# Optimization experiments

Hardware: AMD Instinct MI355X
Metric: run time of the kernel (lower is better)

Reference implementation:

```python
import jax, jax.numpy as jnp
import numpy as np

N_NODES = 50000
N_EDGES = 800000
D_IN = 128
D_HID = 128
D_OUT = 1
N_LAYERS = 3


def _sage_conv(x, src, dst, Wl, bl, Wr):
    # PyG SAGEConv (mean aggr): out = lin_l(mean_{j in N(i)} x_j) + lin_r(x_i)
    n = x.shape[0]
    msg = x[src]                                              # [E, F] gather
    s = jax.ops.segment_sum(msg, dst, num_segments=n)         # [N, F]
    cnt = jax.ops.segment_sum(jnp.ones((src.shape[0],), x.dtype), dst, num_segments=n)
    mean = s / jnp.maximum(cnt, 1.0)[:, None]
    return mean @ Wl.T + bl + x @ Wr.T


def setup_inputs() -> dict:
    key = jax.random.key(0)
    ks = jax.random.split(key, 2 + 3 * N_LAYERS + 2)
    x = jax.random.normal(ks[0], (N_NODES, D_IN), dtype=jnp.float32)
    edge_index = jax.random.randint(ks[1], (2, N_EDGES), 0, N_NODES, dtype=jnp.int64)
    inp = {"x": x, "edge_index": edge_index}
    dims_in = [D_IN] + [D_HID] * (N_LAYERS - 1)
    for i in range(N_LAYERS):
        fi = dims_in[i]
        sc = 1.0 / np.sqrt(fi)
        inp[f"Wl{i}"] = jax.random.uniform(ks[2 + 3 * i], (D_HID, fi), jnp.float32, -sc, sc)
        inp[f"bl{i}"] = jax.random.uniform(ks[3 + 3 * i], (D_HID,), jnp.float32, -sc, sc)
        inp[f"Wr{i}"] = jax.random.uniform(ks[4 + 3 * i], (D_HID, fi), jnp.float32, -sc, sc)
    sc = 1.0 / np.sqrt(D_HID)
    inp["Wf"] = jax.random.uniform(ks[-2], (D_OUT, D_HID), jnp.float32, -sc, sc)
    inp["bf"] = jax.random.uniform(ks[-1], (D_OUT,), jnp.float32, -sc, sc)
    return inp


def reference(x, edge_index, Wl0, bl0, Wr0, Wl1, bl1, Wr1, Wl2, bl2, Wr2, Wf, bf):
    src, dst = edge_index[0], edge_index[1]
    h = x
    # dropout is identity in eval mode (F.dropout with training=False)
    for Wl, bl, Wr in ((Wl0, bl0, Wr0), (Wl1, bl1, Wr1), (Wl2, bl2, Wr2)):
        h = jax.nn.relu(_sage_conv(h, src, dst, Wl, bl, Wr))
    return h @ Wf.T + bf
```

## Files before the change

kernel.cpp:

```cpp
#include <hip/hip_runtime.h>
#include <hip/hip_bf16.h>


constexpr int NN = 50000;
constexpr int NE = 800000;
constexpr int NTILE = NN / 16;
constexpr int EPB = 4096;
constexpr int NBLK = (NE + EPB - 1) / EPB;
constexpr int NBUCK = 196;
constexpr int BCAP = 6144;
constexpr int PCAP = 6144;
constexpr int GGRID = 512;
constexpr int XBLK = (NN * 128 / 4 + 255) / 256;

using bf16x8 = __attribute__((ext_vector_type(8))) short;
using f32x4  = __attribute__((ext_vector_type(4))) float;

__device__ __forceinline__ unsigned short bf16_rne(float f) {
    unsigned u = __float_as_uint(f);
    unsigned r = (u + 0x7FFFu + ((u >> 16) & 1u)) >> 16;
    return (unsigned short)r;
}
__device__ __forceinline__ float bf16_f(unsigned short h) {
    return __uint_as_float(((unsigned)h) << 16);
}
__device__ __forceinline__ unsigned pack_split(float v) {
    unsigned short hi = bf16_rne(v);
    float r = v - bf16_f(hi);
    unsigned short lo = bf16_rne(r);
    return (((unsigned)hi) << 16) | (unsigned)lo;
}


__global__ __launch_bounds__(256) void k_packinit(const float* __restrict__ x,
        unsigned short* __restrict__ hhi, unsigned short* __restrict__ hlo,
        float* __restrict__ out, const float* __restrict__ bf,
        int* __restrict__ bcnt,
        const float* __restrict__ Wl0, const float* __restrict__ Wr0,
        const float* __restrict__ Wl1, const float* __restrict__ Wr1,
        const float* __restrict__ Wl2, const float* __restrict__ Wr2,
        unsigned short* __restrict__ whi, unsigned short* __restrict__ wlo) {
    if (blockIdx.x >= XBLK) {
        int gi = (blockIdx.x - XBLK) * 256 + threadIdx.x;
        int layer = gi >> 15;
        int i = gi & 32767;
        const float* Wl = (layer == 0) ? Wl0 : (layer == 1) ? Wl1 : Wl2;
        const float* Wr = (layer == 0) ? Wr0 : (layer == 1) ? Wr1 : Wr2;
        int c = i >> 8;
        int k = i & 255;
        float v = (k < 128) ? Wl[c * 128 + k] : Wr[c * 128 + (k - 128)];
        unsigned short hi = bf16_rne(v);
        whi[gi] = hi;
        wlo[gi] = bf16_rne(v - bf16_f(hi));
        return;
    }
    int i = blockIdx.x * blockDim.x + threadIdx.x;
    constexpr int TOT = NN * 128 / 4;
    if (i < TOT) {
        float4 v = ((const float4*)x)[i];
        unsigned p0 = pack_split(v.x), p1 = pack_split(v.y);
        unsigned p2 = pack_split(v.z), p3 = pack_split(v.w);
        uint2 hi, lo;
        hi.x = (p0 >> 16) | (p1 & 0xFFFF0000u);
        hi.y = (p2 >> 16) | (p3 & 0xFFFF0000u);
        lo.x = (p0 & 0xFFFFu) | (p1 << 16);
        lo.y = (p2 & 0xFFFFu) | (p3 << 16);
        ((uint2*)hhi)[i] = hi;
        ((uint2*)hlo)[i] = lo;
    }
    if (i < NN) out[i] = bf[0];
    if (i < 256) bcnt[i] = 0;
    if (i < 128) hhi[(size_t)NN * 128 + i] = 0;
}


__global__ __launch_bounds__(256) void k_build_buckets(const int* __restrict__ ei,
        int* __restrict__ bcnt, unsigned* __restrict__ packed) {
    __shared__ unsigned stage[EPB];
    __shared__ int h[256];
    __shared__ int cur[256];
    int t = threadIdx.x;
    h[t] = 0;
    __syncthreads();
    int e0 = blockIdx.x * EPB;
    int e1 = e0 + EPB; if (e1 > NE) e1 = NE;
    for (int e = e0 + t; e < e1; e += 256) {
        int s = ei[e];
        int d = ei[NE + e];
        stage[e - e0] = ((unsigned)d << 16) | (unsigned)s;
        atomicAdd(&h[d >> 8], 1);
    }
    __syncthreads();
    if (t < NBUCK) cur[t] = t * BCAP + atomicAdd(&bcnt[t], h[t]);
    __syncthreads();
    for (int e = e0 + t; e < e1; e += 256) {
        unsigned r = stage[e - e0];
        int pos = atomicAdd(&cur[r >> 24], 1);
        packed[pos] = r;
    }
}

__global__ __launch_bounds__(256) void k_bucket_csr(const unsigned* __restrict__ packed,
        const int* __restrict__ bcnt, unsigned short* __restrict__ perm,
        int* __restrict__ cnt, int* __restrict__ row_start) {
    __shared__ unsigned recs[BCAP];
    __shared__ unsigned short outs[PCAP];
    __shared__ int cntL[256];
    __shared__ int ws[4];
    __shared__ int totS;
    int b = blockIdx.x;
    int m = bcnt[b];
    if (m > BCAP) m = BCAP;
    int t = threadIdx.x;
    cntL[t] = 0;
    __syncthreads();
    int lo = b * BCAP;
    for (int i = t; i < m; i += 256) {
        unsigned r = packed[lo + i];
        recs[i] = r;
        atomicAdd(&cntL[(r >> 16) & 255], 1);
    }
    __syncthreads();
    int lane = t & 63, wave = t >> 6;
    int orig = cntL[t];
    int pc = (orig + 7) & ~7;
    int v = pc;
    for (int o = 1; o < 64; o <<= 1) { int u = __shfl_up(v, o); if (lane >= o) v += u; }
    if (lane == 63) ws[wave] = v;
    __syncthreads();
    int off = 0;
    for (int w = 0; w < wave; ++w) off += ws[w];
    int st = v + off - pc;
    int node = b * 256 + t;
    if (node < NN) { cnt[node] = orig; row_start[node] = b * PCAP + st; }
    if (t == 255) totS = st + pc;
    __syncthreads();
    cntL[t] = st;
    __syncthreads();
    for (int i = t; i < m; i += 256) {
        unsigned r = recs[i];
        int pos = atomicAdd(&cntL[(r >> 16) & 255], 1);
        outs[pos] = (unsigned short)(r & 0xFFFFu);
    }
    for (int i = st + orig; i < st + pc; ++i) outs[i] = (unsigned short)NN;
    __syncthreads();
    int totp = totS;
    for (int i = t; i < totp; i += 256)
        perm[b * PCAP + i] = outs[i];
}

__global__ __launch_bounds__(256) void k_aggregate(const unsigned short* __restrict__ hhi,
        const int* __restrict__ row_start, const int* __restrict__ cnt,
        const unsigned short* __restrict__ perm,
        unsigned short* __restrict__ shi) {
    int wave = __builtin_amdgcn_readfirstlane(threadIdx.x >> 6);
    int lane = threadIdx.x & 63;
    int node = blockIdx.x * 4 + wave;
    if (node >= NN) return;
    int deg = cnt[node];
    int start = row_start[node];
    int eg = lane >> 4;
    int hsh = (eg & 1) << 4;
    bool egHi = (eg & 2) != 0;
    int c16 = (lane & 15) << 4;
    const char* base = (const char*)hhi;
    float a0=0.f,a1=0.f,a2=0.f,a3=0.f,a4=0.f,a5=0.f,a6=0.f,a7=0.f;
#define ACC8(q) { a0 += __uint_as_float((q).x << 16); a1 += __uint_as_float((q).x & 0xFFFF0000u); \
                  a2 += __uint_as_float((q).y << 16); a3 += __uint_as_float((q).y & 0xFFFF0000u); \
                  a4 += __uint_as_float((q).z << 16); a5 += __uint_as_float((q).z & 0xFFFF0000u); \
                  a6 += __uint_as_float((q).w << 16); a7 += __uint_as_float((q).w & 0xFFFF0000u); }
#define GATH(w) (*(const uint4*)(base + ((size_t)(((w) >> hsh) & 0xFFFFu) << 8) + c16))
    int pdeg = (deg + 7) & ~7;
    const uint4* pp = (const uint4*)(perm + start);
    int j = 0;
    for (; j + 16 <= pdeg; j += 16) {
        uint4 P0 = pp[0], P1 = pp[1]; pp += 2;
        unsigned w0 = egHi ? P0.y : P0.x;
        unsigned w1 = egHi ? P0.w : P0.z;
        unsigned w2 = egHi ? P1.y : P1.x;
        unsigned w3 = egHi ? P1.w : P1.z;
        uint4 q0 = GATH(w0);
        uint4 q1 = GATH(w1);
        uint4 q2 = GATH(w2);
        uint4 q3 = GATH(w3);
        ACC8(q0); ACC8(q1); ACC8(q2); ACC8(q3);
    }
    if (j < pdeg) {
        uint4 P0 = *pp;
        unsigned w0 = egHi ? P0.y : P0.x;
        unsigned w1 = egHi ? P0.w : P0.z;
        uint4 q0 = GATH(w0);
        uint4 q1 = GATH(w1);
        ACC8(q0); ACC8(q1);
    }
#undef GATH
#undef ACC8
    a0 += __shfl_xor(a0, 16); a1 += __shfl_xor(a1, 16);
    a2 += __shfl_xor(a2, 16); a3 += __shfl_xor(a3, 16);
    a4 += __shfl_xor(a4, 16); a5 += __shfl_xor(a5, 16);
    a6 += __shfl_xor(a6, 16); a7 += __shfl_xor(a7, 16);
    a0 += __shfl_xor(a0, 32); a1 += __shfl_xor(a1, 32);
    a2 += __shfl_xor(a2, 32); a3 += __shfl_xor(a3, 32);
    a4 += __shfl_xor(a4, 32); a5 += __shfl_xor(a5, 32);
    a6 += __shfl_xor(a6, 32); a7 += __shfl_xor(a7, 32);
    float inv = 1.0f / (float)(deg > 1 ? deg : 1);
    if (eg == 0) {
        uint4 o;
        o.x = (unsigned)bf16_rne(a0 * inv) | ((unsigned)bf16_rne(a1 * inv) << 16);
        o.y = (unsigned)bf16_rne(a2 * inv) | ((unsigned)bf16_rne(a3 * inv) << 16);
        o.z = (unsigned)bf16_rne(a4 * inv) | ((unsigned)bf16_rne(a5 * inv) << 16);
        o.w = (unsigned)bf16_rne(a6 * inv) | ((unsigned)bf16_rne(a7 * inv) << 16);
        ((uint4*)shi)[(size_t)node * 16 + (lane & 15)] = o;
    }
}

#define GEMM_PROLOG \
    int wave = __builtin_amdgcn_readfirstlane(threadIdx.x >> 6); \
    int lane = threadIdx.x & 63; \
    int row = lane & 15; \
    int kb = lane >> 4; \
    int ct0 = wave * 2; \
    bf16x8 bh[2][8], bl[2][8]; \
    _Pragma("unroll") \
    for (int c = 0; c < 2; ++c) \
        _Pragma("unroll") \
        for (int kc = 0; kc < 8; ++kc) { \
            size_t widx = (size_t)((ct0 + c) * 16 + row) * 256 + kc * 32 + kb * 8; \
            bh[c][kc] = *(const bf16x8*)(Whi + widx); \
            bl[c][kc] = *(const bf16x8*)(Wlo + widx); \
        } \
    float b0 = bias[ct0 * 16 + row]; \
    float b1 = bias[ct0 * 16 + 16 + row];

#define LOADT(AS, AH, AL, t) { \
        size_t rb = (size_t)((t) * 16 + row) * 128 + kb * 8; \
        _Pragma("unroll") \
        for (int kc = 0; kc < 4; ++kc) { \
            AS[kc] = *(const bf16x8*)(Ash + rb + kc * 32); \
            AH[kc] = *(const bf16x8*)(Ahh + rb + kc * 32); \
            AL[kc] = *(const bf16x8*)(Ahl + rb + kc * 32); \
        } }

#define MFMA40(AS, AH, AL) \
        f32x4 acc0 = {0.f, 0.f, 0.f, 0.f}; \
        f32x4 acc1 = {0.f, 0.f, 0.f, 0.f}; \
        _Pragma("unroll") \
        for (int kc = 0; kc < 4; ++kc) { \
            acc0 = __builtin_amdgcn_mfma_f32_16x16x32_bf16(AS[kc], bh[0][kc], acc0, 0, 0, 0); \
            acc0 = __builtin_amdgcn_mfma_f32_16x16x32_bf16(AS[kc], bl[0][kc], acc0, 0, 0, 0); \
            acc1 = __builtin_amdgcn_mfma_f32_16x16x32_bf16(AS[kc], bh[1][kc], acc1, 0, 0, 0); \
            acc1 = __builtin_amdgcn_mfma_f32_16x16x32_bf16(AS[kc], bl[1][kc], acc1, 0, 0, 0); \
        } \
        _Pragma("unroll") \
        for (int kc = 0; kc < 4; ++kc) { \
            acc0 = __builtin_amdgcn_mfma_f32_16x16x32_bf16(AH[kc], bh[0][4 + kc], acc0, 0, 0, 0); \
            acc0 = __builtin_amdgcn_mfma_f32_16x16x32_bf16(AL[kc], bh[0][4 + kc], acc0, 0, 0, 0); \
            acc0 = __builtin_amdgcn_mfma_f32_16x16x32_bf16(AH[kc], bl[0][4 + kc], acc0, 0, 0, 0); \
            acc1 = __builtin_amdgcn_mfma_f32_16x16x32_bf16(AH[kc], bh[1][4 + kc], acc1, 0, 0, 0); \
            acc1 = __builtin_amdgcn_mfma_f32_16x16x32_bf16(AL[kc], bh[1][4 + kc], acc1, 0, 0, 0); \
            acc1 = __builtin_amdgcn_mfma_f32_16x16x32_bf16(AH[kc], bl[1][4 + kc], acc1, 0, 0, 0); \
        }

__global__ __launch_bounds__(256, 2) void k_gemm_ws(
        const unsigned short* __restrict__ Ash,
        const unsigned short* __restrict__ Ahh, const unsigned short* __restrict__ Ahl,
        const unsigned short* __restrict__ Whi, const unsigned short* __restrict__ Wlo,
        const float* __restrict__ bias,
        unsigned short* __restrict__ Ohi, unsigned short* __restrict__ Olo) {
    GEMM_PROLOG
#define STEP(AS, AH, AL, t) { \
        MFMA40(AS, AH, AL) \
        __syncthreads();    \
        int cb0 = ct0 * 16 + row; \
        _Pragma("unroll") \
        for (int r = 0; r < 4; ++r) { \
            size_t ro = (size_t)((t) * 16 + kb * 4 + r) * 128; \
            unsigned p0 = pack_split(fmaxf(acc0[r] + b0, 0.f)); \
            unsigned p1 = pack_split(fmaxf(acc1[r] + b1, 0.f)); \
            Ohi[ro + cb0]      = (unsigned short)(p0 >> 16); \
            Olo[ro + cb0]      = (unsigned short)(p0 & 0xFFFFu); \
            Ohi[ro + cb0 + 16] = (unsigned short)(p1 >> 16); \
            Olo[ro + cb0 + 16] = (unsigned short)(p1 & 0xFFFFu); \
        } }
    bf16x8 sA[4], hA[4], lA[4], sB[4], hB[4], lB[4];
    int t = blockIdx.x;
    LOADT(sA, hA, lA, t)
    int tn = t + GGRID;
    for (;;) {
        if (tn < NTILE) LOADT(sB, hB, lB, tn)
        STEP(sA, hA, lA, t)
        if (tn >= NTILE) break;
        t = tn; tn += GGRID;
        if (tn < NTILE) LOADT(sA, hA, lA, tn)
        STEP(sB, hB, lB, t)
        if (tn >= NTILE) break;
        t = tn; tn += GGRID;
    }
#undef STEP
}

__global__ __launch_bounds__(256, 2) void k_gemm_head(
        const unsigned short* __restrict__ Ash,
        const unsigned short* __restrict__ Ahh, const unsigned short* __restrict__ Ahl,
        const unsigned short* __restrict__ Whi, const unsigned short* __restrict__ Wlo,
        const float* __restrict__ bias, const float* __restrict__ Wf,
        float* __restrict__ out) {
    GEMM_PROLOG
    float w0 = Wf[ct0 * 16 + row];
    float w1 = Wf[ct0 * 16 + 16 + row];
#define HSTEP(AS, AH, AL, t) { \
        MFMA40(AS, AH, AL) \
        float part[4]; \
        _Pragma("unroll") \
        for (int r = 0; r < 4; ++r) \
            part[r] = fmaxf(acc0[r] + b0, 0.f) * w0 + fmaxf(acc1[r] + b1, 0.f) * w1; \
        _Pragma("unroll") \
        for (int o = 1; o < 16; o <<= 1) { \
            _Pragma("unroll") \
            for (int r = 0; r < 4; ++r) part[r] += __shfl_xor(part[r], o); \
        } \
        if (row == 0) { \
            _Pragma("unroll") \
            for (int r = 0; r < 4; ++r) atomicAdd(&out[(t) * 16 + kb * 4 + r], part[r]); \
        } }
    bf16x8 sA[4], hA[4], lA[4], sB[4], hB[4], lB[4];
    int t = blockIdx.x;
    LOADT(sA, hA, lA, t)
    int tn = t + GGRID;
    for (;;) {
        if (tn < NTILE) LOADT(sB, hB, lB, tn)
        HSTEP(sA, hA, lA, t)
        if (tn >= NTILE) break;
        t = tn; tn += GGRID;
        if (tn < NTILE) LOADT(sA, hA, lA, tn)
        HSTEP(sB, hB, lB, t)
        if (tn >= NTILE) break;
        t = tn; tn += GGRID;
    }
#undef HSTEP
}

extern "C" void kernel_launch(void* const* d_in, const int* in_sizes, int n_in,
                              void* d_out, int out_size, void* d_ws, size_t ws_size,
                              hipStream_t stream) {
    const float* x   = (const float*)d_in[0];
    const int*   ei  = (const int*)d_in[1];
    const float* Wl0 = (const float*)d_in[2];
    const float* bl0 = (const float*)d_in[3];
    const float* Wr0 = (const float*)d_in[4];
    const float* Wl1 = (const float*)d_in[5];
    const float* bl1 = (const float*)d_in[6];
    const float* Wr1 = (const float*)d_in[7];
    const float* Wl2 = (const float*)d_in[8];
    const float* bl2 = (const float*)d_in[9];
    const float* Wr2 = (const float*)d_in[10];
    const float* Wf  = (const float*)d_in[11];
    const float* bf  = (const float*)d_in[12];
    float* out = (float*)d_out;

    char* p = (char*)d_ws;
    auto alloc = [&](size_t n) { void* r = (void*)p; p += (n + 255) & ~(size_t)255; return r; };
    int*            bcnt      = (int*)alloc(256 * 4);
    int*            cnt       = (int*)alloc((size_t)NN * 4);
    int*            row_start = (int*)alloc((size_t)NN * 4);
    unsigned short* perm      = (unsigned short*)alloc((size_t)NBUCK * PCAP * 2);
    unsigned short* s_hi      = (unsigned short*)alloc((size_t)(NN + 1) * 128 * 2);
    unsigned short* h_hi      = (unsigned short*)alloc((size_t)(NN + 1) * 128 * 2);
    unsigned short* h_lo      = (unsigned short*)alloc((size_t)(NN + 1) * 128 * 2);
    unsigned short* whi       = (unsigned short*)alloc((size_t)3 * 128 * 256 * 2);
    unsigned short* wlo       = (unsigned short*)alloc((size_t)3 * 128 * 256 * 2);
    unsigned*       packed    = (unsigned*)s_hi;

    dim3 b256(256);
    k_packinit<<<dim3(XBLK + 384), b256, 0, stream>>>(
        x, h_hi, h_lo, out, bf, bcnt,
        Wl0, Wr0, Wl1, Wr1, Wl2, Wr2, whi, wlo);
    k_build_buckets<<<dim3(NBLK), b256, 0, stream>>>(ei, bcnt, packed);
    k_bucket_csr<<<dim3(NBUCK), b256, 0, stream>>>(packed, bcnt, perm, cnt, row_start);

    dim3 gAgg((NN + 3) / 4);
    dim3 gGemm(GGRID);

    k_aggregate<<<gAgg, b256, 0, stream>>>(h_hi, row_start, cnt, perm, s_hi);
    k_gemm_ws<<<gGemm, b256, 0, stream>>>(s_hi, h_hi, h_lo,
                                          whi + 0 * 32768, wlo + 0 * 32768, bl0, h_hi, h_lo);
    k_aggregate<<<gAgg, b256, 0, stream>>>(h_hi, row_start, cnt, perm, s_hi);
    k_gemm_ws<<<gGemm, b256, 0, stream>>>(s_hi, h_hi, h_lo,
                                          whi + 1 * 32768, wlo + 1 * 32768, bl1, h_hi, h_lo);
    k_aggregate<<<gAgg, b256, 0, stream>>>(h_hi, row_start, cnt, perm, s_hi);
    k_gemm_head<<<gGemm, b256, 0, stream>>>(s_hi, h_hi, h_lo,
                                            whi + 2 * 32768, wlo + 2 * 32768, bl2, Wf, out);
}
```

Measured before the change: 284.3 us.

## Split aggregate gather into two feature halves over a persistent grid-stride loop

The aggregation kernel now runs as a persistent grid of fixed size. Each wave walks nodes in a grid-stride loop, processing the 128 features in two 128-byte halves. Within a half, 8 lanes cover the 8 chunks of a row and 8 edge groups handle 8 edges at once, so each wave has more independent edges in flight but gathers narrower rows. The aim is to raise memory-level parallelism and keep a smaller working set of feature data resident in cache per pass. In exchange, the perm/cnt/row_start metadata is read twice and an extra shuffle reduction stage is added.

```diff
diff --git a/kernel.cpp b/kernel.cpp
--- a/kernel.cpp
+++ b/kernel.cpp
@@ -11,6 +11,7 @@
 constexpr int BCAP = 6144;
 constexpr int PCAP = 6144;
 constexpr int GGRID = 512;
+constexpr int AGRID = 2048;
 constexpr int XBLK = (NN * 128 / 4 + 255) / 256;
 
 using bf16x8 = __attribute__((ext_vector_type(8))) short;
@@ -155,63 +156,67 @@
         unsigned short* __restrict__ shi) {
     int wave = __builtin_amdgcn_readfirstlane(threadIdx.x >> 6);
     int lane = threadIdx.x & 63;
-    int node = blockIdx.x * 4 + wave;
-    if (node >= NN) return;
-    int deg = cnt[node];
-    int start = row_start[node];
-    int eg = lane >> 4;
+    int eg = lane >> 3;
+    int cl = lane & 7;
     int hsh = (eg & 1) << 4;
-    bool egHi = (eg & 2) != 0;
-    int c16 = (lane & 15) << 4;
+    int wsel = eg >> 1;
     const char* base = (const char*)hhi;
-    float a0=0.f,a1=0.f,a2=0.f,a3=0.f,a4=0.f,a5=0.f,a6=0.f,a7=0.f;
+#define PICK(P) ((((wsel & 2) ? ((wsel & 1) ? (P).w : (P).z) \
+                              : ((wsel & 1) ? (P).y : (P).x)) >> hsh) & 0xFFFFu)
 #define ACC8(q) { a0 += __uint_as_float((q).x << 16); a1 += __uint_as_float((q).x & 0xFFFF0000u); \
                   a2 += __uint_as_float((q).y << 16); a3 += __uint_as_float((q).y & 0xFFFF0000u); \
                   a4 += __uint_as_float((q).z << 16); a5 += __uint_as_float((q).z & 0xFFFF0000u); \
                   a6 += __uint_as_float((q).w << 16); a7 += __uint_as_float((q).w & 0xFFFF0000u); }
-#define GATH(w) (*(const uint4*)(base + ((size_t)(((w) >> hsh) & 0xFFFFu) << 8) + c16))
-    int pdeg = (deg + 7) & ~7;
-    const uint4* pp = (const uint4*)(perm + start);
-    int j = 0;
-    for (; j + 16 <= pdeg; j += 16) {
-        uint4 P0 = pp[0], P1 = pp[1]; pp += 2;
-        unsigned w0 = egHi ? P0.y : P0.x;
-        unsigned w1 = egHi ? P0.w : P0.z;
-        unsigned w2 = egHi ? P1.y : P1.x;
-        unsigned w3 = egHi ? P1.w : P1.z;
-        uint4 q0 = GATH(w0);
-        uint4 q1 = GATH(w1);
-        uint4 q2 = GATH(w2);
-        uint4 q3 = GATH(w3);
-        ACC8(q0); ACC8(q1); ACC8(q2); ACC8(q3);
-    }
-    if (j < pdeg) {
-        uint4 P0 = *pp;
-        unsigned w0 = egHi ? P0.y : P0.x;
-        unsigned w1 = egHi ? P0.w : P0.z;
-        uint4 q0 = GATH(w0);
-        uint4 q1 = GATH(w1);
-        ACC8(q0); ACC8(q1);
-    }
+    for (int p = 0; p < 2; ++p) {
+        int cbyte = p * 128 + cl * 16;
+#define GATH(w) (*(const uint4*)(base + ((size_t)(w) << 8) + cbyte))
+        for (int node = blockIdx.x * 4 + wave; node < NN; node += AGRID * 4) {
+            int deg = cnt[node];
+            int start = row_start[node];
+            float a0=0.f,a1=0.f,a2=0.f,a3=0.f,a4=0.f,a5=0.f,a6=0.f,a7=0.f;
+            int nIter = ((deg + 7) & ~7) >> 3;
+            const uint4* pp = (const uint4*)(perm + start);
+            int j = 0;
+            for (; j + 2 <= nIter; j += 2) {
+                uint4 P0 = pp[j], P1 = pp[j + 1];
+                unsigned w0 = PICK(P0);
+                unsigned w1 = PICK(P1);
+                uint4 q0 = GATH(w0);
+                uint4 q1 = GATH(w1);
+                ACC8(q0); ACC8(q1);
+            }
+            if (j < nIter) {
+                uint4 P0 = pp[j];
+                unsigned w0 = PICK(P0);
+                uint4 q0 = GATH(w0);
+                ACC8(q0);
+            }
+            a0 += __shfl_xor(a0, 8);  a1 += __shfl_xor(a1, 8);
+            a2 += __shfl_xor(a2, 8);  a3 += __shfl_xor(a3, 8);
+            a4 += __shfl_xor(a4, 8);  a5 += __shfl_xor(a5, 8);
+            a6 += __shfl_xor(a6, 8);  a7 += __shfl_xor(a7, 8);
+            a0 += __shfl_xor(a0, 16); a1 += __shfl_xor(a1, 16);
+            a2 += __shfl_xor(a2, 16); a3 += __shfl_xor(a3, 16);
+            a4 += __shfl_xor(a4, 16); a5 += __shfl_xor(a5, 16);
+            a6 += __shfl_xor(a6, 16); a7 += __shfl_xor(a7, 16);
+            a0 += __shfl_xor(a0, 32); a1 += __shfl_xor(a1, 32);
+            a2 += __shfl_xor(a2, 32); a3 += __shfl_xor(a3, 32);
+            a4 += __shfl_xor(a4, 32); a5 += __shfl_xor(a5, 32);
+            a6 += __shfl_xor(a6, 32); a7 += __shfl_xor(a7, 32);
+            float inv = 1.0f / (float)(deg > 1 ? deg : 1);
+            if (eg == 0) {
+                uint4 o;
+                o.x = (unsigned)bf16_rne(a0 * inv) | ((unsigned)bf16_rne(a1 * inv) << 16);
+                o.y = (unsigned)bf16_rne(a2 * inv) | ((unsigned)bf16_rne(a3 * inv) << 16);
+                o.z = (unsigned)bf16_rne(a4 * inv) | ((unsigned)bf16_rne(a5 * inv) << 16);
+                o.w = (unsigned)bf16_rne(a6 * inv) | ((unsigned)bf16_rne(a7 * inv) << 16);
+                ((uint4*)shi)[(size_t)node * 16 + p * 8 + cl] = o;
+            }
+        }
 #undef GATH
+    }
 #undef ACC8
-    a0 += __shfl_xor(a0, 16); a1 += __shfl_xor(a1, 16);
-    a2 += __shfl_xor(a2, 16); a3 += __shfl_xor(a3, 16);
-    a4 += __shfl_xor(a4, 16); a5 += __shfl_xor(a5, 16);
-    a6 += __shfl_xor(a6, 16); a7 += __shfl_xor(a7, 16);
-    a0 += __shfl_xor(a0, 32); a1 += __shfl_xor(a1, 32);
-    a2 += __shfl_xor(a2, 32); a3 += __shfl_xor(a3, 32);
-    a4 += __shfl_xor(a4, 32); a5 += __shfl_xor(a5, 32);
-    a6 += __shfl_xor(a6, 32); a7 += __shfl_xor(a7, 32);
-    float inv = 1.0f / (float)(deg > 1 ? deg : 1);
-    if (eg == 0) {
-        uint4 o;
-        o.x = (unsigned)bf16_rne(a0 * inv) | ((unsigned)bf16_rne(a1 * inv) << 16);
-        o.y = (unsigned)bf16_rne(a2 * inv) | ((unsigned)bf16_rne(a3 * inv) << 16);
-        o.z = (unsigned)bf16_rne(a4 * inv) | ((unsigned)bf16_rne(a5 * inv) << 16);
-        o.w = (unsigned)bf16_rne(a6 * inv) | ((unsigned)bf16_rne(a7 * inv) << 16);
-        ((uint4*)shi)[(size_t)node * 16 + (lane & 15)] = o;
-    }
+#undef PICK
 }
 
 #define GEMM_PROLOG \
@@ -378,7 +383,7 @@
     k_build_buckets<<<dim3(NBLK), b256, 0, stream>>>(ei, bcnt, packed);
     k_bucket_csr<<<dim3(NBUCK), b256, 0, stream>>>(packed, bcnt, perm, cnt, row_start);
 
-    dim3 gAgg((NN + 3) / 4);
+    dim3 gAgg(AGRID);
     dim3 gGemm(GGRID);
 
     k_aggregate<<<gAgg, b256, 0, stream>>>(h_hi, row_start, cnt, perm, s_hi);
```

Measured after the change: 310.4 us. 9.2% more time.
